# Performance work log

Hardware: AMD Instinct MI355X
Metric: run time of the kernel (lower is better)

Reference implementation:

```python
import jax, jax.numpy as jnp
import numpy as np

N, E, DIN, DOUT = 50000, 800000, 64, 64


def setup_inputs() -> dict:
    key = jax.random.key(0)
    k1, k2, k3, k4, k5 = jax.random.split(key, 5)
    x = jax.random.normal(k1, (N, DIN), dtype=jnp.float32)
    edge_index = jax.random.randint(k2, (2, E), 0, N, dtype=jnp.int64)
    edge_attr = jax.random.uniform(k3, (E,), dtype=jnp.float32)
    # PyG GCNConv params: linear weight (no bias in lin) + conv bias
    W = jax.random.normal(k4, (DIN, DOUT), dtype=jnp.float32) / np.sqrt(DIN)
    b = jax.random.normal(k5, (DOUT,), dtype=jnp.float32) * 0.01
    return {
        "x": x,
        "edge_index": edge_index,
        "edge_attr": edge_attr,
        "return_attention_weights": 0,
        "W": W,
        "b": b,
    }


def reference(x, edge_index, edge_attr, return_attention_weights, W, b):
    # GCNConv(add_self_loops=False, normalize=True), edge_weight = ones.
    # edge_attr / return_attention_weights are unused by the original module.
    n = x.shape[0]
    src, dst = edge_index[0], edge_index[1]
    # in-degree on destination nodes (gcn_norm with ones edge weights)
    deg = jax.ops.segment_sum(jnp.ones_like(src, dtype=x.dtype), dst, num_segments=n)
    dis = jnp.where(deg > 0, jax.lax.rsqrt(jnp.maximum(deg, 1)), jnp.zeros_like(deg))
    norm = dis[src] * dis[dst]  # [E]
    h = x @ W  # [N, DOUT] -- transform before aggregation (in < out would flip, equal here)
    msg = h[src] * norm[:, None]  # [E, DOUT]
    out = jax.ops.segment_sum(msg, dst, num_segments=n) + b  # [N, DOUT]
    return out
```

## Files before the change

kernel.cpp:

```cpp
#include <hip/hip_runtime.h>
#include <stdint.h>


#define CAP   64
#define BSH   7
#define NBMAX 512
#define EPB   4096
#define BCAP  2816

typedef float vf4 __attribute__((ext_vector_type(4)));

__device__ __forceinline__ int probe_is64(const void* eidx, int n_edges, int n_nodes) {
    int lane = threadIdx.x & 63;
    const long long* p = (const long long*)eidx;
    int cnt = n_edges < 64 ? n_edges : 64;
    long long v = p[lane % cnt];
    bool ok = (v >= 0) && (v < (long long)n_nodes);
    return (__ballot(ok) == ~0ull) ? 1 : 0;
}

__device__ __forceinline__ int load_idx(const void* eidx, long long i, int is64) {
    if (is64) return (int)((const long long*)eidx)[i];
    return ((const int*)eidx)[i];
}

__device__ __forceinline__ unsigned short f2bf(float v) {
    unsigned u = __float_as_uint(v);
    unsigned r = (u + 0x7fffu + ((u >> 16) & 1u)) >> 16;
    return (unsigned short)r;
}

__device__ __forceinline__ float bflo(unsigned u) { return __uint_as_float(u << 16); }
__device__ __forceinline__ float bfhi(unsigned u) { return __uint_as_float(u & 0xffff0000u); }

__global__ __launch_bounds__(256) void k_front2(
    const float* __restrict__ x, const float* __restrict__ W,
    unsigned* __restrict__ h32w,
    const void* eidx, unsigned* __restrict__ tails,
    unsigned* __restrict__ buckets,
    int n, int ne, int nb, int binb)
{
    union SM {
        struct { unsigned histo[NBMAX]; unsigned base[NBMAX]; } bin;
        struct { float Ws[64 * 64]; float xs[64 * 68]; } gm;
    };
    __shared__ SM sm;
    const int tid = (int)threadIdx.x;
    const int bid = (int)blockIdx.x;

    if (bid < binb) {
        for (int i = tid; i < NBMAX; i += 256) sm.bin.histo[i] = 0u;
        int is64 = probe_is64(eidx, ne, n);
        __syncthreads();

        unsigned pk[16], rk[16];
        long long e0 = (long long)bid * EPB + tid;
        #pragma unroll
        for (int j = 0; j < 16; ++j) {
            long long e = e0 + 256 * j;
            if (e < (long long)ne) {
                int s = load_idx(eidx, e, is64);
                int t = load_idx(eidx, (long long)ne + e, is64);
                pk[j] = ((unsigned)t << 16) | (unsigned)s;
                rk[j] = atomicAdd(&sm.bin.histo[(unsigned)t >> BSH], 1u);
            } else { pk[j] = 0u; rk[j] = 0xFFFFFFFFu; }
        }
        __syncthreads();
        unsigned U = tails[NBMAX];
        for (int b2 = tid; b2 < nb; b2 += 256) {
            unsigned cc = sm.bin.histo[b2];
            sm.bin.base[b2] = cc ? (atomicAdd(&tails[b2], cc) - U) : 0u;
        }
        __syncthreads();
        #pragma unroll
        for (int j = 0; j < 16; ++j) {
            if (rk[j] != 0xFFFFFFFFu) {
                unsigned bk = pk[j] >> (16 + BSH);
                unsigned slot = sm.bin.base[bk] + rk[j];
                if (slot < (unsigned)BCAP)
                    buckets[(size_t)bk * BCAP + slot] = pk[j];
            }
        }
        return;
    }

    const int row0 = (bid - binb) * 64;
    for (int j = 0; j < 4; ++j) {
        int q = tid + 256 * j;
        float4 w4 = ((const float4*)W)[q];
        float* d = &sm.gm.Ws[q * 4];
        d[0] = w4.x; d[1] = w4.y; d[2] = w4.z; d[3] = w4.w;
    }
    for (int j = 0; j < 4; ++j) {
        int q = tid + 256 * j;
        int r = q >> 4, c4 = (q & 15) * 4;
        int row = row0 + r;
        float4 v4 = (row < n) ? ((const float4*)x)[(size_t)row * 16 + (q & 15)]
                              : make_float4(0.f, 0.f, 0.f, 0.f);
        float* d = &sm.gm.xs[r * 68 + c4];
        d[0] = v4.x; d[1] = v4.y; d[2] = v4.z; d[3] = v4.w;
    }
    __syncthreads();

    const int fg = tid & 15, rg = tid >> 4;
    const int r0 = rg * 4;
    float acc[4][4];
    #pragma unroll
    for (int i = 0; i < 4; ++i)
        #pragma unroll
        for (int j = 0; j < 4; ++j) acc[i][j] = 0.f;

    #pragma unroll 4
    for (int k = 0; k < 64; ++k) {
        vf4 w4 = *(const vf4*)&sm.gm.Ws[k * 64 + fg * 4];
        float x0 = sm.gm.xs[(r0 + 0) * 68 + k];
        float x1 = sm.gm.xs[(r0 + 1) * 68 + k];
        float x2 = sm.gm.xs[(r0 + 2) * 68 + k];
        float x3 = sm.gm.xs[(r0 + 3) * 68 + k];
        acc[0][0] += x0 * w4.x; acc[0][1] += x0 * w4.y; acc[0][2] += x0 * w4.z; acc[0][3] += x0 * w4.w;
        acc[1][0] += x1 * w4.x; acc[1][1] += x1 * w4.y; acc[1][2] += x1 * w4.z; acc[1][3] += x1 * w4.w;
        acc[2][0] += x2 * w4.x; acc[2][1] += x2 * w4.y; acc[2][2] += x2 * w4.z; acc[2][3] += x2 * w4.w;
        acc[3][0] += x3 * w4.x; acc[3][1] += x3 * w4.y; acc[3][2] += x3 * w4.z; acc[3][3] += x3 * w4.w;
    }
    #pragma unroll
    for (int i = 0; i < 4; ++i) {
        int row = row0 + r0 + i;
        if (row < n) {
            h32w[(size_t)row * 32 + fg * 2] =
                (unsigned)f2bf(acc[i][0]) | ((unsigned)f2bf(acc[i][1]) << 16);
            h32w[(size_t)row * 32 + fg * 2 + 1] =
                (unsigned)f2bf(acc[i][2]) | ((unsigned)f2bf(acc[i][3]) << 16);
        }
    }
}

__global__ __launch_bounds__(256) void k_place2(
    const unsigned* __restrict__ tails,
    const unsigned* __restrict__ buckets,
    unsigned short* __restrict__ csr16,
    float* __restrict__ dis, unsigned char* __restrict__ endc, int n)
{
    __shared__ unsigned degL[1 << BSH];
    const int tid = (int)threadIdx.x;
    const int b = (int)blockIdx.x;
    const int t0 = b << BSH;
    if (tid < (1 << BSH)) degL[tid] = 0u;
    __syncthreads();
    unsigned U = tails[NBMAX];
    unsigned cnt = tails[b] - U;
    if (cnt > (unsigned)BCAP) cnt = (unsigned)BCAP;
    for (unsigned i = (unsigned)tid; i < cnt; i += 256) {
        unsigned p = buckets[(size_t)b * BCAP + i];
        unsigned dl = (p >> 16) & ((1u << BSH) - 1);
        unsigned r = atomicAdd(&degL[dl], 1u);
        if (r < (unsigned)CAP)
            csr16[((size_t)(t0 + (int)dl)) * CAP + r] = (unsigned short)(p & 0xFFFFu);
    }
    __syncthreads();
    if (tid < (1 << BSH)) {
        int node = t0 + tid;
        if (node < n) {
            unsigned d = degL[tid];
            dis[node] = d ? rsqrtf((float)d) : 0.f;
            endc[node] = (unsigned char)(d < (unsigned)CAP ? d : (unsigned)CAP);
        }
    }
}

__global__ __launch_bounds__(256) void k_place_direct(
    const void* eidx, unsigned* __restrict__ deg,
    unsigned short* __restrict__ csr16, int n, int ne)
{
    int is64 = probe_is64(eidx, ne, n);
    unsigned base = deg[n];
    int e = (int)blockIdx.x * 256 + (int)threadIdx.x;
    if (e >= ne) return;
    int s = load_idx(eidx, e, is64);
    int t = load_idx(eidx, (long long)ne + e, is64);
    unsigned r = atomicAdd(&deg[t], 1u) - base;
    if (r < (unsigned)CAP)
        csr16[(size_t)t * CAP + r] = (unsigned short)s;
}

__global__ __launch_bounds__(256) void k_finalize_direct(
    const unsigned* __restrict__ deg,
    float* __restrict__ dis, unsigned char* __restrict__ endc, int n)
{
    int i = (int)blockIdx.x * 256 + (int)threadIdx.x;
    if (i >= n) return;
    unsigned base = deg[n];
    unsigned cnt = deg[i] - base;
    dis[i] = cnt ? rsqrtf((float)cnt) : 0.f;
    endc[i] = (unsigned char)(cnt < (unsigned)CAP ? cnt : (unsigned)CAP);
}

__global__ __launch_bounds__(256) void k_aggregate(
    const float* __restrict__ dis,
    const unsigned char* __restrict__ endc,
    const unsigned short* __restrict__ csr16,
    const uint2* __restrict__ h64,
    const float* __restrict__ bias,
    float* __restrict__ out, int n)
{
    int wid  = (int)threadIdx.x >> 6;
    int lane = (int)threadIdx.x & 63;
    int t = (int)blockIdx.x * 4 + wid;
    if (t >= n) return;
    int allsrc = (int)csr16[(size_t)t * CAP + lane];
    unsigned end = endc[t];
    float dis_t = dis[t];
    int f = lane & 15, q = lane >> 4;
    float a0 = 0.f, a1 = 0.f, a2 = 0.f, a3 = 0.f;

    unsigned K4 = end >> 4;
    for (unsigned k = 0; k < K4; ++k) {
        int j = q + (int)(k << 4);
        int s0 = __shfl(allsrc, j, 64);
        int s1 = __shfl(allsrc, j + 4, 64);
        int s2 = __shfl(allsrc, j + 8, 64);
        int s3 = __shfl(allsrc, j + 12, 64);
        float w0 = dis[s0], w1 = dis[s1], w2 = dis[s2], w3 = dis[s3];
        uint2 u0 = h64[(size_t)s0 * 16 + f];
        uint2 u1 = h64[(size_t)s1 * 16 + f];
        uint2 u2 = h64[(size_t)s2 * 16 + f];
        uint2 u3 = h64[(size_t)s3 * 16 + f];
        a0 += w0 * bflo(u0.x) + w1 * bflo(u1.x) + w2 * bflo(u2.x) + w3 * bflo(u3.x);
        a1 += w0 * bfhi(u0.x) + w1 * bfhi(u1.x) + w2 * bfhi(u2.x) + w3 * bfhi(u3.x);
        a2 += w0 * bflo(u0.y) + w1 * bflo(u1.y) + w2 * bflo(u2.y) + w3 * bflo(u3.y);
        a3 += w0 * bfhi(u0.y) + w1 * bfhi(u1.y) + w2 * bfhi(u2.y) + w3 * bfhi(u3.y);
    }
    unsigned rem = end & 15u;
    if (rem) {
        unsigned jb = K4 << 4;
        for (unsigned k = 0; k < 4; ++k) {
            unsigned jj = jb + (k << 2) + (unsigned)q;
            bool valid = jj < end;
            int s = __shfl(allsrc, (int)(jj & 63u), 64);
            s = valid ? s : 0;
            float w = valid ? dis[s] : 0.f;
            uint2 u = h64[(size_t)s * 16 + f];
            a0 += w * bflo(u.x);
            a1 += w * bfhi(u.x);
            a2 += w * bflo(u.y);
            a3 += w * bfhi(u.y);
        }
    }
    a0 += __shfl_xor(a0, 16, 64); a0 += __shfl_xor(a0, 32, 64);
    a1 += __shfl_xor(a1, 16, 64); a1 += __shfl_xor(a1, 32, 64);
    a2 += __shfl_xor(a2, 16, 64); a2 += __shfl_xor(a2, 32, 64);
    a3 += __shfl_xor(a3, 16, 64); a3 += __shfl_xor(a3, 32, 64);
    if (q == 0) {
        float4 bb = ((const float4*)bias)[f];
        float4 o;
        o.x = a0 * dis_t + bb.x;
        o.y = a1 * dis_t + bb.y;
        o.z = a2 * dis_t + bb.z;
        o.w = a3 * dis_t + bb.w;
        ((float4*)out)[(size_t)t * 16 + f] = o;
    }
}

extern "C" void kernel_launch(void* const* d_in, const int* in_sizes, int n_in,
                              void* d_out, int out_size, void* d_ws, size_t ws_size,
                              hipStream_t stream) {
    const float* x   = (const float*)d_in[0];
    const void* eidx = d_in[1];
    const float* W   = (const float*)d_in[4];
    const float* b   = (const float*)d_in[5];
    float* out       = (float*)d_out;

    const int n  = in_sizes[0] / 64;
    const int ne = in_sizes[2];
    const int nb = (n + (1 << BSH) - 1) >> BSH;
    const int nchunks = (ne + EPB - 1) / EPB;
    const int ngemm = (n + 63) / 64;

    auto al = [](size_t v) { return (v + 255) & ~(size_t)255; };

    size_t need = al((size_t)(NBMAX + 1) * 4) + al((size_t)nb * BCAP * 4)
                + al((size_t)n * CAP * 2) + al((size_t)n * 32 * 4)
                + al((size_t)n * 4) + al((size_t)n);
    bool binned = (ws_size >= need) && (nb <= NBMAX);

    char* base = (char*)d_ws;
    size_t off = 0;
    unsigned*       tails   = (unsigned*)(base + off);       off = al(off + (size_t)(NBMAX + 1) * 4);
    unsigned*       buckets = (unsigned*)(base + off);       off = al(off + (size_t)nb * BCAP * 4);
    unsigned short* csr16   = (unsigned short*)(base + off); off = al(off + (size_t)n * CAP * 2);
    unsigned*       h32     = (unsigned*)(base + off);       off = al(off + (size_t)n * 32 * 4);
    float*          dis     = (float*)(base + off);          off = al(off + (size_t)n * 4);
    unsigned char*  endc    = (unsigned char*)(base + off);  off = al(off + (size_t)n);

    if (binned) {
        k_front2<<<nchunks + ngemm, 256, 0, stream>>>(x, W, h32, eidx, tails, buckets,
                                                      n, ne, nb, nchunks);
        k_place2<<<nb, 256, 0, stream>>>(tails, buckets, csr16, dis, endc, n);
    } else {
        unsigned* deg = buckets;
        k_front2<<<ngemm, 256, 0, stream>>>(x, W, h32, eidx, tails, buckets,
                                            n, ne, nb, 0);
        k_place_direct<<<(ne + 255) / 256, 256, 0, stream>>>(eidx, deg, csr16, n, ne);
        k_finalize_direct<<<(n + 255) / 256, 256, 0, stream>>>(deg, dis, endc, n);
    }
    k_aggregate<<<(n + 3) / 4, 256, 0, stream>>>(dis, endc, csr16, (const uint2*)h32, b, out, n);
}
```

Measured before the change: 116.6 us.

## Process two destination nodes per wavefront and rebalance binning/placement block sizes

The aggregation kernel now has each wavefront handle two destination nodes, interleaving their gathers so more independent memory loads are in flight per wave, and the launch grid is halved. The binning chunk size is halved to create more front-end blocks, and the placement kernel uses 512 threads per block. The interleaving targets gather latency but adds register pressure and divergence when the two nodes have different degrees.

```diff
diff --git a/kernel.cpp b/kernel.cpp
--- a/kernel.cpp
+++ b/kernel.cpp
@@ -5,7 +5,7 @@
 #define CAP   64
 #define BSH   7
 #define NBMAX 512
-#define EPB   4096
+#define EPB   2048
 #define BCAP  2816
 
 typedef float vf4 __attribute__((ext_vector_type(4)));
@@ -53,10 +53,10 @@
         int is64 = probe_is64(eidx, ne, n);
         __syncthreads();
 
-        unsigned pk[16], rk[16];
+        unsigned pk[8], rk[8];
         long long e0 = (long long)bid * EPB + tid;
         #pragma unroll
-        for (int j = 0; j < 16; ++j) {
+        for (int j = 0; j < 8; ++j) {
             long long e = e0 + 256 * j;
             if (e < (long long)ne) {
                 int s = load_idx(eidx, e, is64);
@@ -73,7 +73,7 @@
         }
         __syncthreads();
         #pragma unroll
-        for (int j = 0; j < 16; ++j) {
+        for (int j = 0; j < 8; ++j) {
             if (rk[j] != 0xFFFFFFFFu) {
                 unsigned bk = pk[j] >> (16 + BSH);
                 unsigned slot = sm.bin.base[bk] + rk[j];
@@ -134,7 +134,7 @@
     }
 }
 
-__global__ __launch_bounds__(256) void k_place2(
+__global__ __launch_bounds__(512) void k_place2(
     const unsigned* __restrict__ tails,
     const unsigned* __restrict__ buckets,
     unsigned short* __restrict__ csr16,
@@ -149,7 +149,7 @@
     unsigned U = tails[NBMAX];
     unsigned cnt = tails[b] - U;
     if (cnt > (unsigned)BCAP) cnt = (unsigned)BCAP;
-    for (unsigned i = (unsigned)tid; i < cnt; i += 256) {
+    for (unsigned i = (unsigned)tid; i < cnt; i += 512) {
         unsigned p = buckets[(size_t)b * BCAP + i];
         unsigned dl = (p >> 16) & ((1u << BSH) - 1);
         unsigned r = atomicAdd(&degL[dl], 1u);
@@ -202,61 +202,112 @@
     const float* __restrict__ bias,
     float* __restrict__ out, int n)
 {
-    int wid  = (int)threadIdx.x >> 6;
-    int lane = (int)threadIdx.x & 63;
-    int t = (int)blockIdx.x * 4 + wid;
-    if (t >= n) return;
-    int allsrc = (int)csr16[(size_t)t * CAP + lane];
-    unsigned end = endc[t];
-    float dis_t = dis[t];
+    const int tid = (int)threadIdx.x;
+    int wid  = tid >> 6;
+    int lane = tid & 63;
+    int tA = (int)blockIdx.x * 8 + wid;
+    int tB = tA + 4;
+    bool vA = tA < n, vB = tB < n;
+    if (!vA) return;
+    int tBc = vB ? tB : 0;
     int f = lane & 15, q = lane >> 4;
-    float a0 = 0.f, a1 = 0.f, a2 = 0.f, a3 = 0.f;
-
-    unsigned K4 = end >> 4;
-    for (unsigned k = 0; k < K4; ++k) {
-        int j = q + (int)(k << 4);
-        int s0 = __shfl(allsrc, j, 64);
-        int s1 = __shfl(allsrc, j + 4, 64);
-        int s2 = __shfl(allsrc, j + 8, 64);
-        int s3 = __shfl(allsrc, j + 12, 64);
-        float w0 = dis[s0], w1 = dis[s1], w2 = dis[s2], w3 = dis[s3];
-        uint2 u0 = h64[(size_t)s0 * 16 + f];
-        uint2 u1 = h64[(size_t)s1 * 16 + f];
-        uint2 u2 = h64[(size_t)s2 * 16 + f];
-        uint2 u3 = h64[(size_t)s3 * 16 + f];
-        a0 += w0 * bflo(u0.x) + w1 * bflo(u1.x) + w2 * bflo(u2.x) + w3 * bflo(u3.x);
-        a1 += w0 * bfhi(u0.x) + w1 * bfhi(u1.x) + w2 * bfhi(u2.x) + w3 * bfhi(u3.x);
-        a2 += w0 * bflo(u0.y) + w1 * bflo(u1.y) + w2 * bflo(u2.y) + w3 * bflo(u3.y);
-        a3 += w0 * bfhi(u0.y) + w1 * bfhi(u1.y) + w2 * bfhi(u2.y) + w3 * bfhi(u3.y);
-    }
-    unsigned rem = end & 15u;
-    if (rem) {
-        unsigned jb = K4 << 4;
+
+    int rowA = (int)csr16[(size_t)tA  * CAP + lane];
+    int rowB = (int)csr16[(size_t)tBc * CAP + lane];
+    unsigned endA = endc[tA];
+    unsigned endB = vB ? endc[tB] : 0u;
+    float dtA = dis[tA];
+    float dtB = vB ? dis[tB] : 0.f;
+
+    float a0A = 0.f, a1A = 0.f, a2A = 0.f, a3A = 0.f;
+    float a0B = 0.f, a1B = 0.f, a2B = 0.f, a3B = 0.f;
+
+    unsigned K4A = endA >> 4, K4B = endB >> 4;
+    unsigned K4m = K4A > K4B ? K4A : K4B;
+    for (unsigned k = 0; k < K4m; ++k) {
+        if (k < K4A) {
+            int j = q + (int)(k << 4);
+            int s0 = __shfl(rowA, j, 64);
+            int s1 = __shfl(rowA, j + 4, 64);
+            int s2 = __shfl(rowA, j + 8, 64);
+            int s3 = __shfl(rowA, j + 12, 64);
+            float w0 = dis[s0], w1 = dis[s1], w2 = dis[s2], w3 = dis[s3];
+            uint2 u0 = h64[(size_t)s0 * 16 + f];
+            uint2 u1 = h64[(size_t)s1 * 16 + f];
+            uint2 u2 = h64[(size_t)s2 * 16 + f];
+            uint2 u3 = h64[(size_t)s3 * 16 + f];
+            a0A += w0 * bflo(u0.x) + w1 * bflo(u1.x) + w2 * bflo(u2.x) + w3 * bflo(u3.x);
+            a1A += w0 * bfhi(u0.x) + w1 * bfhi(u1.x) + w2 * bfhi(u2.x) + w3 * bfhi(u3.x);
+            a2A += w0 * bflo(u0.y) + w1 * bflo(u1.y) + w2 * bflo(u2.y) + w3 * bflo(u3.y);
+            a3A += w0 * bfhi(u0.y) + w1 * bfhi(u1.y) + w2 * bfhi(u2.y) + w3 * bfhi(u3.y);
+        }
+        if (k < K4B) {
+            int j = q + (int)(k << 4);
+            int s0 = __shfl(rowB, j, 64);
+            int s1 = __shfl(rowB, j + 4, 64);
+            int s2 = __shfl(rowB, j + 8, 64);
+            int s3 = __shfl(rowB, j + 12, 64);
+            float w0 = dis[s0], w1 = dis[s1], w2 = dis[s2], w3 = dis[s3];
+            uint2 u0 = h64[(size_t)s0 * 16 + f];
+            uint2 u1 = h64[(size_t)s1 * 16 + f];
+            uint2 u2 = h64[(size_t)s2 * 16 + f];
+            uint2 u3 = h64[(size_t)s3 * 16 + f];
+            a0B += w0 * bflo(u0.x) + w1 * bflo(u1.x) + w2 * bflo(u2.x) + w3 * bflo(u3.x);
+            a1B += w0 * bfhi(u0.x) + w1 * bfhi(u1.x) + w2 * bfhi(u2.x) + w3 * bfhi(u3.x);
+            a2B += w0 * bflo(u0.y) + w1 * bflo(u1.y) + w2 * bflo(u2.y) + w3 * bflo(u3.y);
+            a3B += w0 * bfhi(u0.y) + w1 * bfhi(u1.y) + w2 * bfhi(u2.y) + w3 * bfhi(u3.y);
+        }
+    }
+    unsigned remA = endA & 15u, remB = endB & 15u;
+    if (remA | remB) {
+        unsigned jbA = K4A << 4, jbB = K4B << 4;
         for (unsigned k = 0; k < 4; ++k) {
-            unsigned jj = jb + (k << 2) + (unsigned)q;
-            bool valid = jj < end;
-            int s = __shfl(allsrc, (int)(jj & 63u), 64);
-            s = valid ? s : 0;
-            float w = valid ? dis[s] : 0.f;
-            uint2 u = h64[(size_t)s * 16 + f];
-            a0 += w * bflo(u.x);
-            a1 += w * bfhi(u.x);
-            a2 += w * bflo(u.y);
-            a3 += w * bfhi(u.y);
-        }
-    }
-    a0 += __shfl_xor(a0, 16, 64); a0 += __shfl_xor(a0, 32, 64);
-    a1 += __shfl_xor(a1, 16, 64); a1 += __shfl_xor(a1, 32, 64);
-    a2 += __shfl_xor(a2, 16, 64); a2 += __shfl_xor(a2, 32, 64);
-    a3 += __shfl_xor(a3, 16, 64); a3 += __shfl_xor(a3, 32, 64);
+            {
+                unsigned jj = jbA + (k << 2) + (unsigned)q;
+                bool valid = jj < endA;
+                int s = __shfl(rowA, (int)(jj & 63u), 64);
+                s = valid ? s : 0;
+                float w = valid ? dis[s] : 0.f;
+                uint2 u = h64[(size_t)s * 16 + f];
+                a0A += w * bflo(u.x); a1A += w * bfhi(u.x);
+                a2A += w * bflo(u.y); a3A += w * bfhi(u.y);
+            }
+            {
+                unsigned jj = jbB + (k << 2) + (unsigned)q;
+                bool valid = vB && (jj < endB);
+                int s = __shfl(rowB, (int)(jj & 63u), 64);
+                s = valid ? s : 0;
+                float w = valid ? dis[s] : 0.f;
+                uint2 u = h64[(size_t)s * 16 + f];
+                a0B += w * bflo(u.x); a1B += w * bfhi(u.x);
+                a2B += w * bflo(u.y); a3B += w * bfhi(u.y);
+            }
+        }
+    }
+    a0A += __shfl_xor(a0A, 16, 64); a0A += __shfl_xor(a0A, 32, 64);
+    a1A += __shfl_xor(a1A, 16, 64); a1A += __shfl_xor(a1A, 32, 64);
+    a2A += __shfl_xor(a2A, 16, 64); a2A += __shfl_xor(a2A, 32, 64);
+    a3A += __shfl_xor(a3A, 16, 64); a3A += __shfl_xor(a3A, 32, 64);
+    a0B += __shfl_xor(a0B, 16, 64); a0B += __shfl_xor(a0B, 32, 64);
+    a1B += __shfl_xor(a1B, 16, 64); a1B += __shfl_xor(a1B, 32, 64);
+    a2B += __shfl_xor(a2B, 16, 64); a2B += __shfl_xor(a2B, 32, 64);
+    a3B += __shfl_xor(a3B, 16, 64); a3B += __shfl_xor(a3B, 32, 64);
     if (q == 0) {
         float4 bb = ((const float4*)bias)[f];
         float4 o;
-        o.x = a0 * dis_t + bb.x;
-        o.y = a1 * dis_t + bb.y;
-        o.z = a2 * dis_t + bb.z;
-        o.w = a3 * dis_t + bb.w;
-        ((float4*)out)[(size_t)t * 16 + f] = o;
+        o.x = a0A * dtA + bb.x;
+        o.y = a1A * dtA + bb.y;
+        o.z = a2A * dtA + bb.z;
+        o.w = a3A * dtA + bb.w;
+        ((float4*)out)[(size_t)tA * 16 + f] = o;
+    } else if (q == 1 && vB) {
+        float4 bb = ((const float4*)bias)[f];
+        float4 o;
+        o.x = a0B * dtB + bb.x;
+        o.y = a1B * dtB + bb.y;
+        o.z = a2B * dtB + bb.z;
+        o.w = a3B * dtB + bb.w;
+        ((float4*)out)[(size_t)tB * 16 + f] = o;
     }
 }
 
@@ -294,7 +345,7 @@
     if (binned) {
         k_front2<<<nchunks + ngemm, 256, 0, stream>>>(x, W, h32, eidx, tails, buckets,
                                                       n, ne, nb, nchunks);
-        k_place2<<<nb, 256, 0, stream>>>(tails, buckets, csr16, dis, endc, n);
+        k_place2<<<nb, 512, 0, stream>>>(tails, buckets, csr16, dis, endc, n);
     } else {
         unsigned* deg = buckets;
         k_front2<<<ngemm, 256, 0, stream>>>(x, W, h32, eidx, tails, buckets,
@@ -302,5 +353,5 @@
         k_place_direct<<<(ne + 255) / 256, 256, 0, stream>>>(eidx, deg, csr16, n, ne);
         k_finalize_direct<<<(n + 255) / 256, 256, 0, stream>>>(deg, dis, endc, n);
     }
-    k_aggregate<<<(n + 3) / 4, 256, 0, stream>>>(dis, endc, csr16, (const uint2*)h32, b, out, n);
-}
+    k_aggregate<<<(n + 7) / 8, 256, 0, stream>>>(dis, endc, csr16, (const uint2*)h32, b, out, n);
+}
```

Result: slower. 124.9 us (+7.1%).

## Fuse CSR build into aggregation via shared-memory per-bucket adjacency

Applied to the files above, without the earlier changes.

Replaces the global CSR placement kernel with a degree-only pass plus an aggregation kernel that rebuilds each bucket's adjacency lists in shared memory and then aggregates directly from them. Bucket size is halved (64 nodes per block, 512 threads) so the local CSR fits in LDS. This removes the global csr16/endc write and re-read traffic. In exchange, every bucket is read twice (once for degrees, once in aggregation), and the dst-bucket binning in the front kernel now has more, smaller buckets.

```diff
diff --git a/kernel.cpp b/kernel.cpp
--- a/kernel.cpp
+++ b/kernel.cpp
@@ -3,10 +3,10 @@
 
 
 #define CAP   64
-#define BSH   7
-#define NBMAX 512
+#define BSH   6
+#define NBMAX 1024
 #define EPB   4096
-#define BCAP  2816
+#define BCAP  1408
 
 typedef float vf4 __attribute__((ext_vector_type(4)));
 
@@ -134,35 +134,119 @@
     }
 }
 
-__global__ __launch_bounds__(256) void k_place2(
+__global__ __launch_bounds__(256) void k_deg(
     const unsigned* __restrict__ tails,
     const unsigned* __restrict__ buckets,
-    unsigned short* __restrict__ csr16,
-    float* __restrict__ dis, unsigned char* __restrict__ endc, int n)
-{
+    float* __restrict__ dis, int n)
+{
+    __shared__ unsigned degL[1 << BSH];
+    const int tid = (int)threadIdx.x;
+    const int b = (int)blockIdx.x;
+    if (tid < (1 << BSH)) degL[tid] = 0u;
+    __syncthreads();
+    unsigned U = tails[NBMAX];
+    unsigned cnt = tails[b] - U;
+    if (cnt > (unsigned)BCAP) cnt = (unsigned)BCAP;
+    const size_t bbase = (size_t)b * BCAP;
+    for (unsigned i = (unsigned)tid; i < cnt; i += 256)
+        atomicAdd(&degL[(buckets[bbase + i] >> 16) & ((1u << BSH) - 1)], 1u);
+    __syncthreads();
+    if (tid < (1 << BSH)) {
+        int node = (b << BSH) + tid;
+        if (node < n) {
+            unsigned d = degL[tid];
+            dis[node] = d ? rsqrtf((float)d) : 0.f;
+        }
+    }
+}
+
+__global__ __launch_bounds__(512) void k_agg3(
+    const unsigned* __restrict__ tails,
+    const unsigned* __restrict__ buckets,
+    const float* __restrict__ dis,
+    const uint2* __restrict__ h64,
+    const float* __restrict__ bias,
+    float* __restrict__ out, int n)
+{
+    __shared__ unsigned short csrL[64 * 64];
     __shared__ unsigned degL[1 << BSH];
     const int tid = (int)threadIdx.x;
     const int b = (int)blockIdx.x;
     const int t0 = b << BSH;
     if (tid < (1 << BSH)) degL[tid] = 0u;
     __syncthreads();
+
     unsigned U = tails[NBMAX];
     unsigned cnt = tails[b] - U;
     if (cnt > (unsigned)BCAP) cnt = (unsigned)BCAP;
-    for (unsigned i = (unsigned)tid; i < cnt; i += 256) {
-        unsigned p = buckets[(size_t)b * BCAP + i];
+    const size_t bbase = (size_t)b * BCAP;
+    for (unsigned i = (unsigned)tid; i < cnt; i += 512) {
+        unsigned p = buckets[bbase + i];
         unsigned dl = (p >> 16) & ((1u << BSH) - 1);
         unsigned r = atomicAdd(&degL[dl], 1u);
         if (r < (unsigned)CAP)
-            csr16[((size_t)(t0 + (int)dl)) * CAP + r] = (unsigned short)(p & 0xFFFFu);
-    }
-    __syncthreads();
-    if (tid < (1 << BSH)) {
-        int node = t0 + tid;
-        if (node < n) {
-            unsigned d = degL[tid];
-            dis[node] = d ? rsqrtf((float)d) : 0.f;
-            endc[node] = (unsigned char)(d < (unsigned)CAP ? d : (unsigned)CAP);
+            csrL[dl * 64 + r] = (unsigned short)(p & 0xFFFFu);
+    }
+    __syncthreads();
+
+    const int wid = tid >> 6, lane = tid & 63;
+    const int f = lane & 15, q = lane >> 4;
+    #pragma unroll 1
+    for (int ii = 0; ii < 8; ++ii) {
+        int nl = wid * 8 + ii;
+        int t = t0 + nl;
+        if (t >= n) continue;
+        unsigned d = degL[nl];
+        unsigned end = d < (unsigned)CAP ? d : (unsigned)CAP;
+        float dis_t = dis[t];
+        int row = (int)csrL[nl * 64 + lane];
+        float a0 = 0.f, a1 = 0.f, a2 = 0.f, a3 = 0.f;
+
+        unsigned K4 = end >> 4;
+        for (unsigned k = 0; k < K4; ++k) {
+            int j = q + (int)(k << 4);
+            int s0 = __shfl(row, j, 64);
+            int s1 = __shfl(row, j + 4, 64);
+            int s2 = __shfl(row, j + 8, 64);
+            int s3 = __shfl(row, j + 12, 64);
+            float w0 = dis[s0], w1 = dis[s1], w2 = dis[s2], w3 = dis[s3];
+            uint2 u0 = h64[(size_t)s0 * 16 + f];
+            uint2 u1 = h64[(size_t)s1 * 16 + f];
+            uint2 u2 = h64[(size_t)s2 * 16 + f];
+            uint2 u3 = h64[(size_t)s3 * 16 + f];
+            a0 += w0 * bflo(u0.x) + w1 * bflo(u1.x) + w2 * bflo(u2.x) + w3 * bflo(u3.x);
+            a1 += w0 * bfhi(u0.x) + w1 * bfhi(u1.x) + w2 * bfhi(u2.x) + w3 * bfhi(u3.x);
+            a2 += w0 * bflo(u0.y) + w1 * bflo(u1.y) + w2 * bflo(u2.y) + w3 * bflo(u3.y);
+            a3 += w0 * bfhi(u0.y) + w1 * bfhi(u1.y) + w2 * bfhi(u2.y) + w3 * bfhi(u3.y);
+        }
+        unsigned rem = end & 15u;
+        if (rem) {
+            unsigned jb = K4 << 4;
+            for (unsigned k = 0; k < 4; ++k) {
+                unsigned jj = jb + (k << 2) + (unsigned)q;
+                bool valid = jj < end;
+                int s = __shfl(row, (int)(jj & 63u), 64);
+                s = valid ? s : 0;
+                float w = valid ? dis[s] : 0.f;
+                uint2 u = h64[(size_t)s * 16 + f];
+                a0 += w * bflo(u.x);
+                a1 += w * bfhi(u.x);
+                a2 += w * bflo(u.y);
+                a3 += w * bfhi(u.y);
+            }
+        }
+        a0 += __shfl_xor(a0, 16, 64); a0 += __shfl_xor(a0, 32, 64);
+        a1 += __shfl_xor(a1, 16, 64); a1 += __shfl_xor(a1, 32, 64);
+        a2 += __shfl_xor(a2, 16, 64); a2 += __shfl_xor(a2, 32, 64);
+        a3 += __shfl_xor(a3, 16, 64); a3 += __shfl_xor(a3, 32, 64);
+        if (q == 0) {
+            float4 bb = ((const float4*)bias)[f];
+            float4 o;
+            o.x = a0 * dis_t + bb.x;
+            o.y = a1 * dis_t + bb.y;
+            o.z = a2 * dis_t + bb.z;
+            o.w = a3 * dis_t + bb.w;
+            ((float4*)out)[(size_t)t * 16 + f] = o;
         }
     }
 }
@@ -194,7 +278,7 @@
     endc[i] = (unsigned char)(cnt < (unsigned)CAP ? cnt : (unsigned)CAP);
 }
 
-__global__ __launch_bounds__(256) void k_aggregate(
+__global__ __launch_bounds__(256) void k_aggregate_csr(
     const float* __restrict__ dis,
     const unsigned char* __restrict__ endc,
     const unsigned short* __restrict__ csr16,
@@ -211,7 +295,6 @@
     float dis_t = dis[t];
     int f = lane & 15, q = lane >> 4;
     float a0 = 0.f, a1 = 0.f, a2 = 0.f, a3 = 0.f;
-
     unsigned K4 = end >> 4;
     for (unsigned k = 0; k < K4; ++k) {
         int j = q + (int)(k << 4);
@@ -278,29 +361,30 @@
     auto al = [](size_t v) { return (v + 255) & ~(size_t)255; };
 
     size_t need = al((size_t)(NBMAX + 1) * 4) + al((size_t)nb * BCAP * 4)
-                + al((size_t)n * CAP * 2) + al((size_t)n * 32 * 4)
-                + al((size_t)n * 4) + al((size_t)n);
+                + al((size_t)n * 32 * 4) + al((size_t)n * 4)
+                + al((size_t)n * CAP * 2) + al((size_t)n);
     bool binned = (ws_size >= need) && (nb <= NBMAX);
 
     char* base = (char*)d_ws;
     size_t off = 0;
     unsigned*       tails   = (unsigned*)(base + off);       off = al(off + (size_t)(NBMAX + 1) * 4);
     unsigned*       buckets = (unsigned*)(base + off);       off = al(off + (size_t)nb * BCAP * 4);
-    unsigned short* csr16   = (unsigned short*)(base + off); off = al(off + (size_t)n * CAP * 2);
     unsigned*       h32     = (unsigned*)(base + off);       off = al(off + (size_t)n * 32 * 4);
     float*          dis     = (float*)(base + off);          off = al(off + (size_t)n * 4);
+    unsigned short* csr16   = (unsigned short*)(base + off); off = al(off + (size_t)n * CAP * 2);
     unsigned char*  endc    = (unsigned char*)(base + off);  off = al(off + (size_t)n);
 
     if (binned) {
         k_front2<<<nchunks + ngemm, 256, 0, stream>>>(x, W, h32, eidx, tails, buckets,
                                                       n, ne, nb, nchunks);
-        k_place2<<<nb, 256, 0, stream>>>(tails, buckets, csr16, dis, endc, n);
+        k_deg<<<nb, 256, 0, stream>>>(tails, buckets, dis, n);
+        k_agg3<<<nb, 512, 0, stream>>>(tails, buckets, dis, (const uint2*)h32, b, out, n);
     } else {
         unsigned* deg = buckets;
         k_front2<<<ngemm, 256, 0, stream>>>(x, W, h32, eidx, tails, buckets,
                                             n, ne, nb, 0);
         k_place_direct<<<(ne + 255) / 256, 256, 0, stream>>>(eidx, deg, csr16, n, ne);
         k_finalize_direct<<<(n + 255) / 256, 256, 0, stream>>>(deg, dis, endc, n);
-    }
-    k_aggregate<<<(n + 3) / 4, 256, 0, stream>>>(dis, endc, csr16, (const uint2*)h32, b, out, n);
-}
+        k_aggregate_csr<<<(n + 3) / 4, 256, 0, stream>>>(dis, endc, csr16, (const uint2*)h32, b, out, n);
+    }
+}
```

Measured after the change: 118.6 us. No clear change (+1.7%).
